# Kernel tuning notes

Hardware: AMD Instinct MI355X
Metric: run time of the kernel (lower is better)

The kernel has to match this reference:

```python
import jax, jax.numpy as jnp
import numpy as np

B, N, D, K = 16, 512, 256, 12  # batch, nodes, node_dim, num edge types (4 arg + 4 arg' + punct +/- + no_edges +/-)
ITERATION_STEPS = 1


def setup_inputs() -> dict:
    key = jax.random.key(0)
    ks = jax.random.split(key, 8)
    node = jax.random.normal(ks[0], (B, N, D), dtype=jnp.float32)
    node_mask = jax.random.randint(ks[1], (B, N), 0, 2, dtype=jnp.int32)
    graphs = jax.random.randint(ks[2], (K, B, N, N), 0, 2, dtype=jnp.int32)
    s = 1.0 / np.sqrt(D)
    Ww = jax.random.normal(ks[3], (1, D), dtype=jnp.float32) * s   # _node_weight_fc
    bw = jnp.zeros((1,), dtype=jnp.float32)
    Ws = jax.random.normal(ks[4], (D, D), dtype=jnp.float32) * s   # _self_node_fc
    bs = jnp.zeros((D,), dtype=jnp.float32)
    Wk = jax.random.normal(ks[5], (K, D, D), dtype=jnp.float32) * s  # 12 bias-free per-edge-type linears
    return {"node": node, "Ww": Ww, "bw": bw, "Ws": Ws, "bs": bs, "Wk": Wk,
            "node_mask": node_mask, "graphs": graphs}


def reference(node, Ww, bw, Ws, bs, Wk, node_mask, graphs):
    dt = node.dtype
    mask = node_mask.astype(dt)
    eye = jnp.eye(N, dtype=dt)
    # dd_graph = mask_row * mask_col * (1 - diag)
    dd = mask[:, None, :] * mask[:, :, None] * (1.0 - eye)          # [B,N,N]
    g = dd[None] * graphs.astype(dt)                                # [K,B,N,N] masked adjacencies
    neigh = g.sum(axis=(0, 3))                                      # [B,N] total neighbor count
    neigh = jnp.where(neigh >= 1, neigh, jnp.ones((), dt))

    all_w = []
    for _ in range(ITERATION_STEPS):
        # (1) node relatedness
        w = jax.nn.sigmoid(node @ Ww.T + bw)[..., 0]                # [B,N]
        all_w.append(w)
        self_info = node @ Ws.T + bs                                # [B,N,D]
        # (2) message propagation for all 12 edge types, batched
        trans = jnp.einsum('bnd,ked->kbne', node, Wk)               # [K,B,N,D] per-type linear (x @ W.T)
        wg = w[None, :, None, :] * g                                # [K,B,N,N] masked node weights
        agg = jnp.einsum('kbmn,kbnd->bmd', wg, trans) / neigh[..., None]
        # (3) update
        node = jax.nn.relu(self_info + agg)

    all_weight = jnp.stack(all_w, axis=1)                           # [B,steps,N]
    return node, all_weight
```

## Files before the change

kernel.cpp:

```cpp
#include <hip/hip_runtime.h>
#include <hip/hip_bf16.h>
#include <math.h>

#define BB 16
#define NN 512
#define DD 256
#define KK 12

typedef __bf16 bf16x8 __attribute__((ext_vector_type(8)));
typedef __bf16 bf16x4 __attribute__((ext_vector_type(4)));
typedef float  f32x4  __attribute__((ext_vector_type(4)));

#define WS_WM     0
#define WS_MASKBF 32768
#define WS_NODEBF 49152
#define WS_NODET  4243456
#define WS_WKBF   8437760
#define WS_WSBF   10010624

#define BAR() do { \
    __builtin_amdgcn_sched_barrier(0); \
    asm volatile("s_waitcnt lgkmcnt(0)" ::: "memory"); \
    __builtin_amdgcn_s_barrier(); \
    __builtin_amdgcn_sched_barrier(0); \
} while (0)

__global__ __launch_bounds__(256) void k1_prep(const float* __restrict__ node,
        const float* __restrict__ Ww, const float* __restrict__ bw,
        const int* __restrict__ node_mask,
        float* __restrict__ wm, __bf16* __restrict__ maskbf,
        __bf16* __restrict__ node_bf, float* __restrict__ all_w) {
    int t = threadIdx.x;
    int lane = t & 63;
    int row = blockIdx.x * 4 + (t >> 6);
    const float4 nv = *(const float4*)(node + (size_t)row * DD + lane * 4);
    const float4 wv = *(const float4*)(Ww + lane * 4);
    float dot = nv.x*wv.x + nv.y*wv.y + nv.z*wv.z + nv.w*wv.w;
    #pragma unroll
    for (int off = 32; off > 0; off >>= 1) dot += __shfl_xor(dot, off);
    float w = 1.0f / (1.0f + expf(-(dot + bw[0])));
    int mk = node_mask[row];
    if (lane == 0) {
        wm[row]     = w * (float)mk;
        all_w[row]  = w;
        maskbf[row] = (__bf16)(float)mk;
    }
    bf16x4 nb = {(__bf16)nv.x, (__bf16)nv.y, (__bf16)nv.z, (__bf16)nv.w};
    *(bf16x4*)(node_bf + (size_t)row * DD + lane * 4) = nb;
}

__global__ __launch_bounds__(256) void k1b_convert(const float* __restrict__ Wk,
        const float* __restrict__ Ws, __bf16* __restrict__ Wk_bf, __bf16* __restrict__ Ws_bf) {
    const int KDD = KK * DD * DD;
    int idx = (blockIdx.x * 256 + threadIdx.x) * 4;
    if (idx < KDD) {
        float4 v = *(const float4*)(Wk + idx);
        bf16x4 o = {(__bf16)v.x, (__bf16)v.y, (__bf16)v.z, (__bf16)v.w};
        *(bf16x4*)(Wk_bf + idx) = o;
    } else {
        int j = idx - KDD;
        if (j < DD * DD) {
            float4 v = *(const float4*)(Ws + j);
            bf16x4 o = {(__bf16)v.x, (__bf16)v.y, (__bf16)v.z, (__bf16)v.w};
            *(bf16x4*)(Ws_bf + j) = o;
        }
    }
}

__global__ __launch_bounds__(256) void k2_transpose(const float* __restrict__ node,
        const float* __restrict__ wm, __bf16* __restrict__ dst) {
    __shared__ float tile[64][65];
    int bx = blockIdx.x;
    int b = bx >> 5; int rest = bx & 31; int nt = rest >> 2; int dt = rest & 3;
    int n0 = nt * 64, d0 = dt * 64;
    int t = threadIdx.x;
    #pragma unroll
    for (int i = 0; i < 16; i++) {
        int idx = i * 256 + t;
        int n = idx >> 6, d = idx & 63;
        tile[n][d] = node[((size_t)(b * NN + n0 + n)) * DD + d0 + d];
    }
    __syncthreads();
    #pragma unroll
    for (int i = 0; i < 16; i++) {
        int idx = i * 256 + t;
        int d = idx >> 6, n = idx & 63;
        float w = wm[b * NN + n0 + n];
        dst[((size_t)(b * DD + d0 + d)) * NN + n0 + n] = (__bf16)(tile[n][d] * w);
    }
}

__global__ __launch_bounds__(512, 2) void k45_fused(const int* __restrict__ graphs,
        const int* __restrict__ node_mask, const __bf16* __restrict__ maskbf,
        const __bf16* __restrict__ node_t, const __bf16* __restrict__ node_bf,
        const __bf16* __restrict__ Wk_bf, const __bf16* __restrict__ Ws_bf,
        const float* __restrict__ bs, float* __restrict__ out) {
    __shared__ __align__(16) __bf16 Abf[2][32][520];
    __shared__ __align__(16) __bf16 Tk[2][32][264];
    __shared__ float cntp[8][32];
    __shared__ float sm[32];
    int bx = blockIdx.x;
    int b  = (bx & 7) + 8 * ((bx >> 3) & 1);
    int mt = bx >> 4;
    int m0 = mt * 32;
    int t = threadIdx.x;
    int lane = t & 63;
    int w = t >> 6;
    int q = lane >> 4;
    int l16 = lane & 15;
    int esub = w * 32;
    int dsub = w * 32;

    int crow = t >> 7;
    int ccol = (t & 127) * 4;

    f32x4 accO[2][2];
    #pragma unroll
    for (int i = 0; i < 2; i++)
        #pragma unroll
        for (int j = 0; j < 2; j++) accO[i][j] = (f32x4){0.f, 0.f, 0.f, 0.f};
    f32x4 accC[2];
    accC[0] = (f32x4){0.f, 0.f, 0.f, 0.f};
    accC[1] = (f32x4){0.f, 0.f, 0.f, 0.f};

    int4 g[8];

#define LOADG(kk_) do { \
        const int4* gb = (const int4*)(graphs + ((size_t)(((kk_) * BB + b) * NN + m0)) * NN); \
        _Pragma("unroll") \
        for (int u = 0; u < 8; u++) g[u] = gb[u * 512 + t]; \
    } while (0)

#define CONVERT(nb_) do { \
        _Pragma("unroll") \
        for (int u = 0; u < 8; u++) { \
            int row = u * 4 + crow; \
            unsigned p0 = (unsigned)g[u].x | ((unsigned)g[u].y << 16); \
            unsigned p1 = (unsigned)g[u].z | ((unsigned)g[u].w << 16); \
            unsigned drel = (unsigned)(m0 + row - ccol); \
            if (drel < 2u)      p0 &= ~(0xFFFFu << (16 * drel)); \
            else if (drel < 4u) p1 &= ~(0xFFFFu << (16 * (drel - 2))); \
            uint2 st; st.x = p0 * 0x3F80u; st.y = p1 * 0x3F80u; \
            *(uint2*)&Abf[nb_][row][ccol] = st; \
        } \
    } while (0)

    LOADG(0);
    CONVERT(0);
    LOADG(1);
    BAR();

    int ac = 0, tc = 0;

    #pragma unroll 1
    for (int k = 0; k < KK; k++) {
        f32x4 accT[2][2];
        #pragma unroll
        for (int i = 0; i < 2; i++)
            #pragma unroll
            for (int jj = 0; jj < 2; jj++) accT[i][jj] = (f32x4){0.f, 0.f, 0.f, 0.f};
        #pragma unroll
        for (int kk = 0; kk < 16; kk++) {
            int n0c = kk * 32;
            bf16x8 af[2], bfr[2];
            #pragma unroll
            for (int fm = 0; fm < 2; fm++)
                af[fm] = *(const bf16x8*)&Abf[ac][fm * 16 + l16][n0c + q * 8];
            #pragma unroll
            for (int fd = 0; fd < 2; fd++)
                bfr[fd] = *(const bf16x8*)(node_t +
                    ((size_t)(b * DD + esub + fd * 16 + l16)) * NN + n0c + q * 8);
            #pragma unroll
            for (int fm = 0; fm < 2; fm++)
                #pragma unroll
                for (int fd = 0; fd < 2; fd++)
                    accT[fm][fd] = __builtin_amdgcn_mfma_f32_16x16x32_bf16(
                        af[fm], bfr[fd], accT[fm][fd], 0, 0, 0);
            if ((kk >> 1) == w) {
                bf16x8 bfm = (bf16x8){0,0,0,0,0,0,0,0};
                if (l16 == 0)
                    bfm = *(const bf16x8*)(maskbf + b * NN + n0c + q * 8);
                accC[0] = __builtin_amdgcn_mfma_f32_16x16x32_bf16(af[0], bfm, accC[0], 0, 0, 0);
                accC[1] = __builtin_amdgcn_mfma_f32_16x16x32_bf16(af[1], bfm, accC[1], 0, 0, 0);
            }
        }

        if (k < KK - 1) CONVERT(ac ^ 1);
        if (k < KK - 2) LOADG(k + 2);

        #pragma unroll
        for (int fm = 0; fm < 2; fm++)
            #pragma unroll
            for (int fd = 0; fd < 2; fd++) {
                int col = esub + fd * 16 + l16;
                #pragma unroll
                for (int r = 0; r < 4; r++)
                    Tk[tc][fm * 16 + q * 4 + r][col] = (__bf16)accT[fm][fd][r];
            }

        BAR();

        #pragma unroll
        for (int ee = 0; ee < 8; ee++) {
            int e0c = ee * 32;
            bf16x8 afT[2], bw2[2];
            #pragma unroll
            for (int fm = 0; fm < 2; fm++)
                afT[fm] = *(const bf16x8*)&Tk[tc][fm * 16 + l16][e0c + q * 8];
            #pragma unroll
            for (int fd = 0; fd < 2; fd++)
                bw2[fd] = *(const bf16x8*)(Wk_bf +
                    ((size_t)(k * DD + dsub + fd * 16 + l16)) * DD + e0c + q * 8);
            #pragma unroll
            for (int fm = 0; fm < 2; fm++)
                #pragma unroll
                for (int fd = 0; fd < 2; fd++)
                    accO[fm][fd] = __builtin_amdgcn_mfma_f32_16x16x32_bf16(
                        afT[fm], bw2[fd], accO[fm][fd], 0, 0, 0);
        }

        ac ^= 1; tc ^= 1;
    }

    if (l16 == 0) {
        #pragma unroll
        for (int fm = 0; fm < 2; fm++)
            #pragma unroll
            for (int r = 0; r < 4; r++)
                cntp[w][fm * 16 + q * 4 + r] = accC[fm][r];
    }
    __syncthreads();
    if (t < 32) {
        float c = 0.0f;
        #pragma unroll
        for (int w8 = 0; w8 < 8; w8++) c += cntp[w8][t];
        int mk = node_mask[b * NN + m0 + t];
        sm[t] = (float)mk / (c >= 0.5f ? c : 1.0f);
    }
    __syncthreads();

    #pragma unroll
    for (int fm = 0; fm < 2; fm++)
        #pragma unroll
        for (int r = 0; r < 4; r++) {
            float s = sm[fm * 16 + q * 4 + r];
            #pragma unroll
            for (int fd = 0; fd < 2; fd++) accO[fm][fd][r] *= s;
        }

    #pragma unroll
    for (int ee = 0; ee < 8; ee++) {
        int e0c = ee * 32;
        bf16x8 afS[2], bwS[2];
        #pragma unroll
        for (int fm = 0; fm < 2; fm++)
            afS[fm] = *(const bf16x8*)(node_bf +
                ((size_t)(b * NN + m0 + fm * 16 + l16)) * DD + e0c + q * 8);
        #pragma unroll
        for (int fd = 0; fd < 2; fd++)
            bwS[fd] = *(const bf16x8*)(Ws_bf +
                ((size_t)(dsub + fd * 16 + l16)) * DD + e0c + q * 8);
        #pragma unroll
        for (int fm = 0; fm < 2; fm++)
            #pragma unroll
            for (int fd = 0; fd < 2; fd++)
                accO[fm][fd] = __builtin_amdgcn_mfma_f32_16x16x32_bf16(
                    afS[fm], bwS[fd], accO[fm][fd], 0, 0, 0);
    }

    #pragma unroll
    for (int fm = 0; fm < 2; fm++)
        #pragma unroll
        for (int fd = 0; fd < 2; fd++) {
            int d = dsub + fd * 16 + l16;
            float bsv = bs[d];
            #pragma unroll
            for (int r = 0; r < 4; r++) {
                int m = m0 + fm * 16 + q * 4 + r;
                float v = accO[fm][fd][r] + bsv;
                out[((size_t)(b * NN + m)) * DD + d] = fmaxf(v, 0.0f);
            }
        }
#undef LOADG
#undef CONVERT
}

extern "C" void kernel_launch(void* const* d_in, const int* in_sizes, int n_in,
                              void* d_out, int out_size, void* d_ws, size_t ws_size,
                              hipStream_t stream) {
    const float* node      = (const float*)d_in[0];
    const float* Ww        = (const float*)d_in[1];
    const float* bw        = (const float*)d_in[2];
    const float* Ws        = (const float*)d_in[3];
    const float* bs        = (const float*)d_in[4];
    const float* Wk        = (const float*)d_in[5];
    const int*   node_mask = (const int*)d_in[6];
    const int*   graphs    = (const int*)d_in[7];
    float* out   = (float*)d_out;
    float* all_w = out + (size_t)BB * NN * DD;

    char* ws = (char*)d_ws;
    float*  wm      = (float*)(ws + WS_WM);
    __bf16* maskbf  = (__bf16*)(ws + WS_MASKBF);
    __bf16* node_bf = (__bf16*)(ws + WS_NODEBF);
    __bf16* node_t  = (__bf16*)(ws + WS_NODET);
    __bf16* Wk_bf   = (__bf16*)(ws + WS_WKBF);
    __bf16* Ws_bf   = (__bf16*)(ws + WS_WSBF);

    k1_prep    <<<2048, 256, 0, stream>>>(node, Ww, bw, node_mask, wm, maskbf, node_bf, all_w);
    k1b_convert<<< 832, 256, 0, stream>>>(Wk, Ws, Wk_bf, Ws_bf);
    k2_transpose<<<512, 256, 0, stream>>>(node, wm, node_t);
    k45_fused  <<< 256, 512, 0, stream>>>(graphs, node_mask, maskbf, node_t, node_bf,
                                          Wk_bf, Ws_bf, bs, out);
}
```

Baseline: 348.8 us.

## Hoist node_t fragments into registers and XOR-swizzle LDS tiles

```diff
diff --git a/kernel.cpp b/kernel.cpp
--- a/kernel.cpp
+++ b/kernel.cpp
@@ -95,10 +95,14 @@
         const __bf16* __restrict__ node_t, const __bf16* __restrict__ node_bf,
         const __bf16* __restrict__ Wk_bf, const __bf16* __restrict__ Ws_bf,
         const float* __restrict__ bs, float* __restrict__ out) {
-    __shared__ __align__(16) __bf16 Abf[2][32][520];
-    __shared__ __align__(16) __bf16 Tk[2][32][264];
+    __shared__ __align__(16) char AbfB[2][32 * 1024];
+    __shared__ __align__(16) char TkB[2][32 * 512];
     __shared__ float cntp[8][32];
     __shared__ float sm[32];
+
+#define ABF(buf_, row_, col_) ((__bf16*)(&AbfB[buf_][(((row_) * 1024 + (col_) * 2) ^ (((row_) & 7) << 4))]))
+#define TKP(buf_, row_, col_) ((__bf16*)(&TkB[buf_][(((row_) * 512 + (col_) * 2) ^ (((row_) & 7) << 4))]))
+
     int bx = blockIdx.x;
     int b  = (bx & 7) + 8 * ((bx >> 3) & 1);
     int mt = bx >> 4;
@@ -114,6 +118,22 @@
     int crow = t >> 7;
     int ccol = (t & 127) * 4;
 
+    bf16x8 bfr[16][2];
+    #pragma unroll
+    for (int kk = 0; kk < 16; kk++)
+        #pragma unroll
+        for (int fd = 0; fd < 2; fd++)
+            bfr[kk][fd] = *(const bf16x8*)(node_t +
+                ((size_t)(b * DD + esub + fd * 16 + l16)) * NN + kk * 32 + q * 8);
+
+    bf16x8 bfm[2];
+    #pragma unroll
+    for (int c = 0; c < 2; c++) {
+        bfm[c] = (bf16x8){0,0,0,0,0,0,0,0};
+        if (l16 == 0)
+            bfm[c] = *(const bf16x8*)(maskbf + b * NN + (w * 2 + c) * 32 + q * 8);
+    }
+
     f32x4 accO[2][2];
     #pragma unroll
     for (int i = 0; i < 2; i++)
@@ -141,7 +161,7 @@
             if (drel < 2u)      p0 &= ~(0xFFFFu << (16 * drel)); \
             else if (drel < 4u) p1 &= ~(0xFFFFu << (16 * (drel - 2))); \
             uint2 st; st.x = p0 * 0x3F80u; st.y = p1 * 0x3F80u; \
-            *(uint2*)&Abf[nb_][row][ccol] = st; \
+            *(uint2*)ABF(nb_, row, ccol) = st; \
         } \
     } while (0)
 
@@ -162,26 +182,19 @@
         #pragma unroll
         for (int kk = 0; kk < 16; kk++) {
             int n0c = kk * 32;
-            bf16x8 af[2], bfr[2];
+            bf16x8 af[2];
             #pragma unroll
             for (int fm = 0; fm < 2; fm++)
-                af[fm] = *(const bf16x8*)&Abf[ac][fm * 16 + l16][n0c + q * 8];
-            #pragma unroll
-            for (int fd = 0; fd < 2; fd++)
-                bfr[fd] = *(const bf16x8*)(node_t +
-                    ((size_t)(b * DD + esub + fd * 16 + l16)) * NN + n0c + q * 8);
+                af[fm] = *(const bf16x8*)ABF(ac, fm * 16 + l16, n0c + q * 8);
             #pragma unroll
             for (int fm = 0; fm < 2; fm++)
                 #pragma unroll
                 for (int fd = 0; fd < 2; fd++)
                     accT[fm][fd] = __builtin_amdgcn_mfma_f32_16x16x32_bf16(
-                        af[fm], bfr[fd], accT[fm][fd], 0, 0, 0);
+                        af[fm], bfr[kk][fd], accT[fm][fd], 0, 0, 0);
             if ((kk >> 1) == w) {
-                bf16x8 bfm = (bf16x8){0,0,0,0,0,0,0,0};
-                if (l16 == 0)
-                    bfm = *(const bf16x8*)(maskbf + b * NN + n0c + q * 8);
-                accC[0] = __builtin_amdgcn_mfma_f32_16x16x32_bf16(af[0], bfm, accC[0], 0, 0, 0);
-                accC[1] = __builtin_amdgcn_mfma_f32_16x16x32_bf16(af[1], bfm, accC[1], 0, 0, 0);
+                accC[0] = __builtin_amdgcn_mfma_f32_16x16x32_bf16(af[0], bfm[kk & 1], accC[0], 0, 0, 0);
+                accC[1] = __builtin_amdgcn_mfma_f32_16x16x32_bf16(af[1], bfm[kk & 1], accC[1], 0, 0, 0);
             }
         }
 
@@ -195,7 +208,7 @@
                 int col = esub + fd * 16 + l16;
                 #pragma unroll
                 for (int r = 0; r < 4; r++)
-                    Tk[tc][fm * 16 + q * 4 + r][col] = (__bf16)accT[fm][fd][r];
+                    *TKP(tc, fm * 16 + q * 4 + r, col) = (__bf16)accT[fm][fd][r];
             }
 
         BAR();
@@ -206,7 +219,7 @@
             bf16x8 afT[2], bw2[2];
             #pragma unroll
             for (int fm = 0; fm < 2; fm++)
-                afT[fm] = *(const bf16x8*)&Tk[tc][fm * 16 + l16][e0c + q * 8];
+                afT[fm] = *(const bf16x8*)TKP(tc, fm * 16 + l16, e0c + q * 8);
             #pragma unroll
             for (int fd = 0; fd < 2; fd++)
                 bw2[fd] = *(const bf16x8*)(Wk_bf +
@@ -283,6 +296,8 @@
         }
 #undef LOADG
 #undef CONVERT
+#undef ABF
+#undef TKP
 }
 
 extern "C" void kernel_launch(void* const* d_in, const int* in_sizes, int n_in,
```

Measured after the change: 535.3 us. +53.5%, slower.

## Precompute per-type transformed nodes in a separate GEMM before aggregation

Applied to the files above, without the earlier changes.

```diff
diff --git a/kernel.cpp b/kernel.cpp
--- a/kernel.cpp
+++ b/kernel.cpp
@@ -17,6 +17,9 @@
 #define WS_NODET  4243456
 #define WS_WKBF   8437760
 #define WS_WSBF   10010624
+#define WS_YT     10174464
+#define YT_BYTES  ((size_t)KK * BB * DD * NN * 2)
+#define WS_NEED_YT (WS_YT + YT_BYTES)
 
 #define BAR() do { \
     __builtin_amdgcn_sched_barrier(0); \
@@ -90,7 +93,230 @@
     }
 }
 
-__global__ __launch_bounds__(512, 2) void k45_fused(const int* __restrict__ graphs,
+__global__ __launch_bounds__(256) void k3_ygemm(const __bf16* __restrict__ node_bf,
+        const __bf16* __restrict__ Wk_bf, const float* __restrict__ wm,
+        __bf16* __restrict__ Yt) {
+    int bx = blockIdx.x;
+    int nt = bx & 15;
+    int kb = bx >> 4;
+    int b  = kb & 15;
+    int k  = kb >> 4;
+    int t = threadIdx.x;
+    int lane = t & 63;
+    int w = t >> 6;
+    int q = lane >> 4;
+    int l16 = lane & 15;
+    int wsub = w * 64;
+
+    f32x4 acc[4][2];
+    #pragma unroll
+    for (int i = 0; i < 4; i++)
+        #pragma unroll
+        for (int j = 0; j < 2; j++) acc[i][j] = (f32x4){0.f, 0.f, 0.f, 0.f};
+
+    #pragma unroll
+    for (int ec = 0; ec < 8; ec++) {
+        int e0 = ec * 32;
+        bf16x8 aW[4], bN[2];
+        #pragma unroll
+        for (int fd = 0; fd < 4; fd++)
+            aW[fd] = *(const bf16x8*)(Wk_bf +
+                ((size_t)(k * DD + wsub + fd * 16 + l16)) * DD + e0 + q * 8);
+        #pragma unroll
+        for (int fn = 0; fn < 2; fn++)
+            bN[fn] = *(const bf16x8*)(node_bf +
+                ((size_t)(b * NN + nt * 32 + fn * 16 + l16)) * DD + e0 + q * 8);
+        #pragma unroll
+        for (int fd = 0; fd < 4; fd++)
+            #pragma unroll
+            for (int fn = 0; fn < 2; fn++)
+                acc[fd][fn] = __builtin_amdgcn_mfma_f32_16x16x32_bf16(
+                    aW[fd], bN[fn], acc[fd][fn], 0, 0, 0);
+    }
+
+    float wmv[2];
+    #pragma unroll
+    for (int fn = 0; fn < 2; fn++)
+        wmv[fn] = wm[b * NN + nt * 32 + fn * 16 + l16];
+
+    #pragma unroll
+    for (int fd = 0; fd < 4; fd++)
+        #pragma unroll
+        for (int fn = 0; fn < 2; fn++) {
+            int n = nt * 32 + fn * 16 + l16;
+            #pragma unroll
+            for (int r = 0; r < 4; r++) {
+                int d = wsub + fd * 16 + q * 4 + r;
+                Yt[((size_t)(k * BB + b) * DD + d) * NN + n] =
+                    (__bf16)(acc[fd][fn][r] * wmv[fn]);
+            }
+        }
+}
+
+__global__ __launch_bounds__(512, 2) void k45_yt(const int* __restrict__ graphs,
+        const int* __restrict__ node_mask, const __bf16* __restrict__ maskbf,
+        const __bf16* __restrict__ Yt, const __bf16* __restrict__ node_bf,
+        const __bf16* __restrict__ Ws_bf,
+        const float* __restrict__ bs, float* __restrict__ out) {
+    __shared__ __align__(16) __bf16 Abf[2][32][520];
+    __shared__ float cntp[8][32];
+    __shared__ float sm[32];
+    int bx = blockIdx.x;
+    int b  = (bx & 7) + 8 * ((bx >> 3) & 1);
+    int mt = bx >> 4;
+    int m0 = mt * 32;
+    int t = threadIdx.x;
+    int lane = t & 63;
+    int w = t >> 6;
+    int q = lane >> 4;
+    int l16 = lane & 15;
+    int dsub = w * 32;
+
+    int crow = t >> 7;
+    int ccol = (t & 127) * 4;
+
+    bf16x8 bfm[2];
+    #pragma unroll
+    for (int c = 0; c < 2; c++) {
+        bfm[c] = (bf16x8){0,0,0,0,0,0,0,0};
+        if (l16 == 0)
+            bfm[c] = *(const bf16x8*)(maskbf + b * NN + (w * 2 + c) * 32 + q * 8);
+    }
+
+    f32x4 accO[2][2];
+    #pragma unroll
+    for (int i = 0; i < 2; i++)
+        #pragma unroll
+        for (int j = 0; j < 2; j++) accO[i][j] = (f32x4){0.f, 0.f, 0.f, 0.f};
+    f32x4 accC[2];
+    accC[0] = (f32x4){0.f, 0.f, 0.f, 0.f};
+    accC[1] = (f32x4){0.f, 0.f, 0.f, 0.f};
+
+    int4 g[8];
+
+#define LOADG(kk_) do { \
+        const int4* gb = (const int4*)(graphs + ((size_t)(((kk_) * BB + b) * NN + m0)) * NN); \
+        _Pragma("unroll") \
+        for (int u = 0; u < 8; u++) g[u] = gb[u * 512 + t]; \
+    } while (0)
+
+#define CONVERT(nb_) do { \
+        _Pragma("unroll") \
+        for (int u = 0; u < 8; u++) { \
+            int row = u * 4 + crow; \
+            unsigned p0 = (unsigned)g[u].x | ((unsigned)g[u].y << 16); \
+            unsigned p1 = (unsigned)g[u].z | ((unsigned)g[u].w << 16); \
+            unsigned drel = (unsigned)(m0 + row - ccol); \
+            if (drel < 2u)      p0 &= ~(0xFFFFu << (16 * drel)); \
+            else if (drel < 4u) p1 &= ~(0xFFFFu << (16 * (drel - 2))); \
+            uint2 st; st.x = p0 * 0x3F80u; st.y = p1 * 0x3F80u; \
+            *(uint2*)&Abf[nb_][row][ccol] = st; \
+        } \
+    } while (0)
+
+    LOADG(0);
+    CONVERT(0);
+    LOADG(1);
+    BAR();
+
+    int ac = 0;
+
+    #pragma unroll 1
+    for (int k = 0; k < KK; k++) {
+        #pragma unroll
+        for (int kk = 0; kk < 16; kk++) {
+            int n0c = kk * 32;
+            bf16x8 af[2], byt[2];
+            #pragma unroll
+            for (int fm = 0; fm < 2; fm++)
+                af[fm] = *(const bf16x8*)&Abf[ac][fm * 16 + l16][n0c + q * 8];
+            #pragma unroll
+            for (int fd = 0; fd < 2; fd++)
+                byt[fd] = *(const bf16x8*)(Yt +
+                    ((size_t)(k * BB + b) * DD + dsub + fd * 16 + l16) * NN + n0c + q * 8);
+            #pragma unroll
+            for (int fm = 0; fm < 2; fm++)
+                #pragma unroll
+                for (int fd = 0; fd < 2; fd++)
+                    accO[fm][fd] = __builtin_amdgcn_mfma_f32_16x16x32_bf16(
+                        af[fm], byt[fd], accO[fm][fd], 0, 0, 0);
+            if ((kk >> 1) == w) {
+                accC[0] = __builtin_amdgcn_mfma_f32_16x16x32_bf16(af[0], bfm[kk & 1], accC[0], 0, 0, 0);
+                accC[1] = __builtin_amdgcn_mfma_f32_16x16x32_bf16(af[1], bfm[kk & 1], accC[1], 0, 0, 0);
+            }
+        }
+
+        if (k < KK - 1) CONVERT(ac ^ 1);
+        if (k < KK - 2) LOADG(k + 2);
+
+        BAR();
+        ac ^= 1;
+    }
+
+    if (l16 == 0) {
+        #pragma unroll
+        for (int fm = 0; fm < 2; fm++)
+            #pragma unroll
+            for (int r = 0; r < 4; r++)
+                cntp[w][fm * 16 + q * 4 + r] = accC[fm][r];
+    }
+    __syncthreads();
+    if (t < 32) {
+        float c = 0.0f;
+        #pragma unroll
+        for (int w8 = 0; w8 < 8; w8++) c += cntp[w8][t];
+        int mk = node_mask[b * NN + m0 + t];
+        sm[t] = (float)mk / (c >= 0.5f ? c : 1.0f);
+    }
+    __syncthreads();
+
+    #pragma unroll
+    for (int fm = 0; fm < 2; fm++)
+        #pragma unroll
+        for (int r = 0; r < 4; r++) {
+            float s = sm[fm * 16 + q * 4 + r];
+            #pragma unroll
+            for (int fd = 0; fd < 2; fd++) accO[fm][fd][r] *= s;
+        }
+
+    #pragma unroll
+    for (int ee = 0; ee < 8; ee++) {
+        int e0c = ee * 32;
+        bf16x8 afS[2], bwS[2];
+        #pragma unroll
+        for (int fm = 0; fm < 2; fm++)
+            afS[fm] = *(const bf16x8*)(node_bf +
+                ((size_t)(b * NN + m0 + fm * 16 + l16)) * DD + e0c + q * 8);
+        #pragma unroll
+        for (int fd = 0; fd < 2; fd++)
+            bwS[fd] = *(const bf16x8*)(Ws_bf +
+                ((size_t)(dsub + fd * 16 + l16)) * DD + e0c + q * 8);
+        #pragma unroll
+        for (int fm = 0; fm < 2; fm++)
+            #pragma unroll
+            for (int fd = 0; fd < 2; fd++)
+                accO[fm][fd] = __builtin_amdgcn_mfma_f32_16x16x32_bf16(
+                    afS[fm], bwS[fd], accO[fm][fd], 0, 0, 0);
+    }
+
+    #pragma unroll
+    for (int fm = 0; fm < 2; fm++)
+        #pragma unroll
+        for (int fd = 0; fd < 2; fd++) {
+            int d = dsub + fd * 16 + l16;
+            float bsv = bs[d];
+            #pragma unroll
+            for (int r = 0; r < 4; r++) {
+                int m = m0 + fm * 16 + q * 4 + r;
+                float v = accO[fm][fd][r] + bsv;
+                out[((size_t)(b * NN + m)) * DD + d] = fmaxf(v, 0.0f);
+            }
+        }
+#undef LOADG
+#undef CONVERT
+}
+
+__global__ __launch_bounds__(512, 2) void k45_r4(const int* __restrict__ graphs,
         const int* __restrict__ node_mask, const __bf16* __restrict__ maskbf,
         const __bf16* __restrict__ node_t, const __bf16* __restrict__ node_bf,
         const __bf16* __restrict__ Wk_bf, const __bf16* __restrict__ Ws_bf,
@@ -306,10 +532,18 @@
     __bf16* node_t  = (__bf16*)(ws + WS_NODET);
     __bf16* Wk_bf   = (__bf16*)(ws + WS_WKBF);
     __bf16* Ws_bf   = (__bf16*)(ws + WS_WSBF);
+    __bf16* Yt      = (__bf16*)(ws + WS_YT);
 
     k1_prep    <<<2048, 256, 0, stream>>>(node, Ww, bw, node_mask, wm, maskbf, node_bf, all_w);
     k1b_convert<<< 832, 256, 0, stream>>>(Wk, Ws, Wk_bf, Ws_bf);
-    k2_transpose<<<512, 256, 0, stream>>>(node, wm, node_t);
-    k45_fused  <<< 256, 512, 0, stream>>>(graphs, node_mask, maskbf, node_t, node_bf,
-                                          Wk_bf, Ws_bf, bs, out);
-}
+
+    if (ws_size >= WS_NEED_YT) {
+        k3_ygemm <<<3072, 256, 0, stream>>>(node_bf, Wk_bf, wm, Yt);
+        k45_yt   <<< 256, 512, 0, stream>>>(graphs, node_mask, maskbf, Yt, node_bf,
+                                            Ws_bf, bs, out);
+    } else {
+        k2_transpose<<<512, 256, 0, stream>>>(node, wm, node_t);
+        k45_r4   <<< 256, 512, 0, stream>>>(graphs, node_mask, maskbf, node_t, node_bf,
+                                            Wk_bf, Ws_bf, bs, out);
+    }
+}
```

After: 435.1 us. 1.25x slower.
